# Kernel tuning notes

Measured on AMD Instinct MI355X. Metric: run time of the kernel, lower is better.

The kernel has to match this reference:

```python
import jax, jax.numpy as jnp
import numpy as np

VOLUME_SIZE = 48  # max_disp / down = 192 / 4


def setup_inputs() -> dict:
    key = jax.random.key(0)
    k1, k2 = jax.random.split(key)
    b, c, h, w = 8, 128, 128, 240
    left_feature = jax.random.normal(k1, (b, c, h, w), dtype=jnp.float32)
    right_feature = jax.random.normal(k2, (b, c, h, w), dtype=jnp.float32)
    return {"left_feature": left_feature, "right_feature": right_feature}


def reference(left_feature, right_feature):
    # cost_volume[:, i, :, x] = mean_c(L[:, :, :, x] * R[:, :, :, x-i]) for x >= i, else 0
    b, c, h, w = left_feature.shape
    col = jnp.arange(w)

    def per_disp(i):
        # shift right feature right by i; zero out wrapped-around columns (< i)
        r_shift = jnp.roll(right_feature, i, axis=-1)  # [b,c,h,w]
        prod_mean = jnp.mean(left_feature * r_shift, axis=1)  # [b,h,w]
        return jnp.where(col >= i, prod_mean, 0.0)

    cv = jax.vmap(per_disp)(jnp.arange(VOLUME_SIZE))  # [V,b,h,w]
    return jnp.transpose(cv, (1, 0, 2, 3))  # [b,V,h,w]
```

## Files before the change

### kernel.cpp

```cpp
#include <hip/hip_runtime.h>
#include <hip/hip_fp16.h>

#define CV_B 8
#define CV_C 128
#define CV_H 128
#define CV_W 240
#define CV_V 48
#define PLANE (CV_H * CV_W)
#define GUARD 48
#define ROWW (GUARD + CV_W)
#define NCP 16
#define NCHUNK 4

__global__ __launch_bounds__(256, 3) void cost_volume_kernel(
        const float* __restrict__ Lf, const float* __restrict__ Rf,
        float* __restrict__ out)
{
    __shared__ __align__(16) __half2 sBuf[2][NCP][ROWW];

    const int t  = threadIdx.x;
    const int y  = blockIdx.x;
    const int b  = blockIdx.y;
    const int wv = t >> 6;
    const int u  = t & 63;
    const bool act = (u < 60);

    const float* Lrow = Lf + (size_t)(b * CV_C) * PLANE + y * CV_W;
    const float* Rrow = Rf + (size_t)(b * CV_C) * PLANE + y * CV_W;

    const int side = wv >> 1;
    const int a0   = (wv & 1) * 8;
    const float* Srow = side ? Rrow : Lrow;

    for (int idx = t; idx < 2 * NCP * GUARD; idx += 256) {
        const int s  = idx / (NCP * GUARD);
        const int rm = idx % (NCP * GUARD);
        sBuf[s][rm / GUARD][rm % GUARD] = __floats2half2_rn(0.f, 0.f);
    }

    float4 f0[8], f1[8];
    if (act) {
#pragma unroll
        for (int q = 0; q < 8; ++q) {
            const float* p = Srow + (size_t)(2 * (a0 + q)) * PLANE + 4 * u;
            f0[q] = *(const float4*)p;
            f1[q] = *(const float4*)(p + PLANE);
        }
#pragma unroll
        for (int q = 0; q < 8; ++q) {
            union { float4 v; __half2 h[4]; } wbuf;
            wbuf.h[0] = __floats2half2_rn(f0[q].x, f1[q].x);
            wbuf.h[1] = __floats2half2_rn(f0[q].y, f1[q].y);
            wbuf.h[2] = __floats2half2_rn(f0[q].z, f1[q].z);
            wbuf.h[3] = __floats2half2_rn(f0[q].w, f1[q].w);
            *(float4*)&sBuf[side][a0 + q][GUARD + 4 * u] = wbuf.v;
        }
    }
    __syncthreads();

    __half2 acc[4][12];
#pragma unroll
    for (int xx = 0; xx < 4; ++xx)
#pragma unroll
        for (int r = 0; r < 12; ++r) acc[xx][r] = __floats2half2_rn(0.f, 0.f);

    const int baseL = GUARD + 4 * u;
    const int baseR = GUARD - 12 - 12 * wv + 4 * u;

    for (int k = 0; k < NCHUNK; ++k) {
        const bool pf = (k + 1 < NCHUNK);
        if (pf && act) {
#pragma unroll
            for (int q = 0; q < 8; ++q) {
                const float* p = Srow + (size_t)((k + 1) * 32 + 2 * (a0 + q)) * PLANE + 4 * u;
                f0[q] = *(const float4*)p;
                f1[q] = *(const float4*)(p + PLANE);
            }
        }

        if (act) {
#pragma unroll
            for (int cp = 0; cp < NCP; ++cp) {
                union { float4 v; __half2 h[4]; } lv, rw[4];
                lv.v = *(const float4*)&sBuf[0][cp][baseL];
#pragma unroll
                for (int kk = 0; kk < 4; ++kk)
                    rw[kk].v = *(const float4*)&sBuf[1][cp][baseR + 4 * kk];
#pragma unroll
                for (int r = 0; r < 12; ++r) {
#pragma unroll
                    for (int xx = 0; xx < 4; ++xx) {
                        const int m = xx + 12 - r;
                        acc[xx][r] = __hfma2(lv.h[xx], rw[m >> 2].h[m & 3], acc[xx][r]);
                    }
                }
            }
        }
        __syncthreads();

        if (pf && act) {
#pragma unroll
            for (int q = 0; q < 8; ++q) {
                union { float4 v; __half2 h[4]; } wbuf;
                wbuf.h[0] = __floats2half2_rn(f0[q].x, f1[q].x);
                wbuf.h[1] = __floats2half2_rn(f0[q].y, f1[q].y);
                wbuf.h[2] = __floats2half2_rn(f0[q].z, f1[q].z);
                wbuf.h[3] = __floats2half2_rn(f0[q].w, f1[q].w);
                *(float4*)&sBuf[side][a0 + q][GUARD + 4 * u] = wbuf.v;
            }
        }
        __syncthreads();
    }

    if (act) {
#pragma unroll
        for (int r = 0; r < 12; ++r) {
            const int i = 12 * wv + r;
            float4 o;
            o.x = (__low2float(acc[0][r]) + __high2float(acc[0][r])) * (1.f / 128.f);
            o.y = (__low2float(acc[1][r]) + __high2float(acc[1][r])) * (1.f / 128.f);
            o.z = (__low2float(acc[2][r]) + __high2float(acc[2][r])) * (1.f / 128.f);
            o.w = (__low2float(acc[3][r]) + __high2float(acc[3][r])) * (1.f / 128.f);
            *(float4*)&out[(((size_t)b * CV_V + i) * CV_H + y) * CV_W + 4 * u] = o;
        }
    }
}

extern "C" void kernel_launch(void* const* d_in, const int* in_sizes, int n_in,
                              void* d_out, int out_size, void* d_ws, size_t ws_size,
                              hipStream_t stream)
{
    const float* Lf = (const float*)d_in[0];
    const float* Rf = (const float*)d_in[1];
    float* o = (float*)d_out;
    dim3 grid(CV_H, CV_B);
    dim3 block(256);
    hipLaunchKernelGGL(cost_volume_kernel, grid, block, 0, stream, Lf, Rf, o);
}
```

Before: 285.7 us.

## Double-buffer smaller shared-memory channel stages with one barrier per stage

Replaces the single shared buffer holding 16 channel pairs per chunk with two ping-pong buffers of 8 channel pairs each, split into separate left and right arrays with a smaller guard region. This drops one of the two barriers per stage, because the next stage's half-precision data is written into the other buffer while the current one is being read. Halving the prefetch registers and the shared footprint allows the occupancy hint to rise from 3 to 4 blocks per SIMD/CU. The cost is twice as many stages, so more loop iterations and barriers overall.

```diff
diff --git a/kernel.cpp b/kernel.cpp
--- a/kernel.cpp
+++ b/kernel.cpp
@@ -7,16 +7,21 @@
 #define CV_W 240
 #define CV_V 48
 #define PLANE (CV_H * CV_W)
-#define GUARD 48
-#define ROWW (GUARD + CV_W)
-#define NCP 16
-#define NCHUNK 4
 
-__global__ __launch_bounds__(256, 3) void cost_volume_kernel(
+#define NCP 8
+#define NSTAGE 8
+#define GUARDF 12
+#define LROW 60
+#define RROW (GUARDF + LROW)
+
+union F4H { float4 v; __half2 h[4]; };
+
+__global__ __launch_bounds__(256, 4) void cost_volume_kernel(
         const float* __restrict__ Lf, const float* __restrict__ Rf,
         float* __restrict__ out)
 {
-    __shared__ __align__(16) __half2 sBuf[2][NCP][ROWW];
+    __shared__ float4 sL[2][NCP][LROW];
+    __shared__ float4 sR[2][NCP][RROW];
 
     const int t  = threadIdx.x;
     const int y  = blockIdx.x;
@@ -24,36 +29,39 @@
     const int wv = t >> 6;
     const int u  = t & 63;
     const bool act = (u < 60);
+    const int x0 = 4 * u;
 
     const float* Lrow = Lf + (size_t)(b * CV_C) * PLANE + y * CV_W;
     const float* Rrow = Rf + (size_t)(b * CV_C) * PLANE + y * CV_W;
 
     const int side = wv >> 1;
-    const int a0   = (wv & 1) * 8;
+    const int a0   = (wv & 1) * 4;
     const float* Srow = side ? Rrow : Lrow;
 
-    for (int idx = t; idx < 2 * NCP * GUARD; idx += 256) {
-        const int s  = idx / (NCP * GUARD);
-        const int rm = idx % (NCP * GUARD);
-        sBuf[s][rm / GUARD][rm % GUARD] = __floats2half2_rn(0.f, 0.f);
+    for (int idx = t; idx < 2 * NCP * GUARDF; idx += 256) {
+        const int bi = idx / (NCP * GUARDF);
+        const int rm = idx % (NCP * GUARDF);
+        sR[bi][rm / GUARDF][rm % GUARDF] = make_float4(0.f, 0.f, 0.f, 0.f);
     }
 
-    float4 f0[8], f1[8];
+    float4 f0[4], f1[4];
+
     if (act) {
 #pragma unroll
-        for (int q = 0; q < 8; ++q) {
-            const float* p = Srow + (size_t)(2 * (a0 + q)) * PLANE + 4 * u;
+        for (int q = 0; q < 4; ++q) {
+            const float* p = Srow + (size_t)(2 * (a0 + q)) * PLANE + x0;
             f0[q] = *(const float4*)p;
             f1[q] = *(const float4*)(p + PLANE);
         }
 #pragma unroll
-        for (int q = 0; q < 8; ++q) {
-            union { float4 v; __half2 h[4]; } wbuf;
-            wbuf.h[0] = __floats2half2_rn(f0[q].x, f1[q].x);
-            wbuf.h[1] = __floats2half2_rn(f0[q].y, f1[q].y);
-            wbuf.h[2] = __floats2half2_rn(f0[q].z, f1[q].z);
-            wbuf.h[3] = __floats2half2_rn(f0[q].w, f1[q].w);
-            *(float4*)&sBuf[side][a0 + q][GUARD + 4 * u] = wbuf.v;
+        for (int q = 0; q < 4; ++q) {
+            F4H w;
+            w.h[0] = __floats2half2_rn(f0[q].x, f1[q].x);
+            w.h[1] = __floats2half2_rn(f0[q].y, f1[q].y);
+            w.h[2] = __floats2half2_rn(f0[q].z, f1[q].z);
+            w.h[3] = __floats2half2_rn(f0[q].w, f1[q].w);
+            if (side) sR[0][a0 + q][GUARDF + u] = w.v;
+            else      sL[0][a0 + q][u]          = w.v;
         }
     }
     __syncthreads();
@@ -64,15 +72,16 @@
 #pragma unroll
         for (int r = 0; r < 12; ++r) acc[xx][r] = __floats2half2_rn(0.f, 0.f);
 
-    const int baseL = GUARD + 4 * u;
-    const int baseR = GUARD - 12 - 12 * wv + 4 * u;
+    const int rbase = GUARDF - 3 - 3 * wv + u;
 
-    for (int k = 0; k < NCHUNK; ++k) {
-        const bool pf = (k + 1 < NCHUNK);
+    for (int s = 0; s < NSTAGE; ++s) {
+        const int P = s & 1;
+        const bool pf = (s + 1 < NSTAGE);
+
         if (pf && act) {
 #pragma unroll
-            for (int q = 0; q < 8; ++q) {
-                const float* p = Srow + (size_t)((k + 1) * 32 + 2 * (a0 + q)) * PLANE + 4 * u;
+            for (int q = 0; q < 4; ++q) {
+                const float* p = Srow + (size_t)(16 * (s + 1) + 2 * (a0 + q)) * PLANE + x0;
                 f0[q] = *(const float4*)p;
                 f1[q] = *(const float4*)(p + PLANE);
             }
@@ -81,11 +90,12 @@
         if (act) {
 #pragma unroll
             for (int cp = 0; cp < NCP; ++cp) {
-                union { float4 v; __half2 h[4]; } lv, rw[4];
-                lv.v = *(const float4*)&sBuf[0][cp][baseL];
+                F4H lv;
+                lv.v = sL[P][cp][u];
+                F4H rw[4];
 #pragma unroll
                 for (int kk = 0; kk < 4; ++kk)
-                    rw[kk].v = *(const float4*)&sBuf[1][cp][baseR + 4 * kk];
+                    rw[kk].v = sR[P][cp][rbase + kk];
 #pragma unroll
                 for (int r = 0; r < 12; ++r) {
 #pragma unroll
@@ -96,20 +106,20 @@
                 }
             }
         }
-        __syncthreads();
 
         if (pf && act) {
 #pragma unroll
-            for (int q = 0; q < 8; ++q) {
-                union { float4 v; __half2 h[4]; } wbuf;
-                wbuf.h[0] = __floats2half2_rn(f0[q].x, f1[q].x);
-                wbuf.h[1] = __floats2half2_rn(f0[q].y, f1[q].y);
-                wbuf.h[2] = __floats2half2_rn(f0[q].z, f1[q].z);
-                wbuf.h[3] = __floats2half2_rn(f0[q].w, f1[q].w);
-                *(float4*)&sBuf[side][a0 + q][GUARD + 4 * u] = wbuf.v;
+            for (int q = 0; q < 4; ++q) {
+                F4H w;
+                w.h[0] = __floats2half2_rn(f0[q].x, f1[q].x);
+                w.h[1] = __floats2half2_rn(f0[q].y, f1[q].y);
+                w.h[2] = __floats2half2_rn(f0[q].z, f1[q].z);
+                w.h[3] = __floats2half2_rn(f0[q].w, f1[q].w);
+                if (side) sR[P ^ 1][a0 + q][GUARDF + u] = w.v;
+                else      sL[P ^ 1][a0 + q][u]          = w.v;
             }
         }
-        __syncthreads();
+        if (pf) __syncthreads();
     }
 
     if (act) {
@@ -121,7 +131,7 @@
             o.y = (__low2float(acc[1][r]) + __high2float(acc[1][r])) * (1.f / 128.f);
             o.z = (__low2float(acc[2][r]) + __high2float(acc[2][r])) * (1.f / 128.f);
             o.w = (__low2float(acc[3][r]) + __high2float(acc[3][r])) * (1.f / 128.f);
-            *(float4*)&out[(((size_t)b * CV_V + i) * CV_H + y) * CV_W + 4 * u] = o;
+            *(float4*)&out[(((size_t)b * CV_V + i) * CV_H + y) * CV_W + x0] = o;
         }
     }
 }
```

After: 285.3 us. About the same (-0.1%).
